# Kernel tuning notes

Hardware: AMD Instinct MI355X
Metric: run time of the kernel (lower is better)

Reference implementation:

```python
import jax, jax.numpy as jnp
import numpy as np
import math

D_MODEL = 2048
N_HEADS = 16
D_FF = 8192
SEQ = 2048
BATCH = 2
THETA = 10000.0
EPS = 1e-5


def _rope(x, pos):
    # x: [B, H, S, d_k] ; pos: [B, S] int
    d = x.shape[-1]
    inv_freq = 1.0 / (THETA ** (jnp.arange(0, d, 2, dtype=jnp.float32) / d))  # [d/2]
    ang = pos[..., None].astype(jnp.float32) * inv_freq  # [B, S, d/2]
    cos = jnp.cos(ang)[:, None, :, :, None]  # [B,1,S,d/2,1]
    sin = jnp.sin(ang)[:, None, :, :, None]
    xr = x.reshape(*x.shape[:-1], d // 2, 2)
    x1, x2 = xr[..., 0], xr[..., 1]
    rot = jnp.stack((-x2, x1), axis=-1)  # rotate pairs
    out = xr * cos + rot * sin
    return out.reshape(x.shape)


def _trunc_normal(key, shape, in_f, out_f):
    std = math.sqrt(2.0 / (in_f + out_f))
    return jax.random.truncated_normal(key, -3.0, 3.0, shape, jnp.float32) * std


def setup_inputs() -> dict:
    key = jax.random.key(0)
    ks = jax.random.split(key, 8)
    x = jax.random.normal(ks[0], (BATCH, SEQ, D_MODEL), jnp.float32)
    token_positions = jnp.sort(jax.random.randint(ks[1], (BATCH, SEQ), 0, SEQ), axis=-1)
    W_qkv = _trunc_normal(ks[2], (3 * D_MODEL, D_MODEL), D_MODEL, 3 * D_MODEL)
    W_o = _trunc_normal(ks[3], (D_MODEL, D_MODEL), D_MODEL, D_MODEL)
    W1 = _trunc_normal(ks[4], (D_FF, D_MODEL), D_MODEL, D_FF)
    W3 = _trunc_normal(ks[5], (D_FF, D_MODEL), D_MODEL, D_FF)
    W2 = _trunc_normal(ks[6], (D_MODEL, D_FF), D_FF, D_MODEL)
    g1 = jnp.ones((D_MODEL,), jnp.float32)
    g2 = jnp.ones((D_MODEL,), jnp.float32)
    return {"x": x, "token_positions": token_positions, "W_qkv": W_qkv, "W_o": W_o,
            "g1": g1, "g2": g2, "W1": W1, "W3": W3, "W2": W2}


def _rmsnorm(x, g):
    xf = x.astype(jnp.float32)
    rms = jnp.sqrt(jnp.mean(xf * xf, axis=-1, keepdims=True) + EPS)
    return (xf / rms * g).astype(x.dtype)


def reference(x, token_positions, W_qkv, W_o, g1, g2, W1, W3, W2):
    B, S, D = x.shape
    H = N_HEADS
    dk = D // H
    # --- attention sublayer ---
    h = _rmsnorm(x, g1)
    qkv = jnp.einsum('bsi,oi->bso', h, W_qkv)  # [B,S,3D]
    q, k, v = jnp.split(qkv, 3, axis=-1)
    to_heads = lambda t: t.reshape(B, S, H, dk).transpose(0, 2, 1, 3)  # [B,H,S,dk]
    q, k, v = to_heads(q), to_heads(k), to_heads(v)
    q = _rope(q, token_positions)
    k = _rope(k, token_positions)
    scores = jnp.einsum('bhnd,bhmd->bhnm', q, k) / math.sqrt(dk)  # [B,H,S,S]
    mask = jnp.tril(jnp.ones((S, S), dtype=bool))
    scores = jnp.where(mask, scores, -jnp.inf)
    attn = jax.nn.softmax(scores, axis=-1)
    o = jnp.einsum('bhnm,bhmd->bhnd', attn, v)
    o = o.transpose(0, 2, 1, 3).reshape(B, S, D)
    x = x + jnp.einsum('bsi,oi->bso', o, W_o)
    # --- SwiGLU FFN sublayer ---
    h2 = _rmsnorm(x, g2)
    x1 = jnp.einsum('bsi,oi->bso', h2, W1)
    x3 = jnp.einsum('bsi,oi->bso', h2, W3)
    x = x + jnp.einsum('bsi,oi->bso', jax.nn.silu(x1) * x3, W2)
    return x
```

## Files before the change

### kernel.cpp

```cpp
#include <hip/hip_runtime.h>

#define DEV __device__ __forceinline__

typedef __bf16 bf16x8 __attribute__((ext_vector_type(8)));
typedef float f32x4 __attribute__((ext_vector_type(4)));
typedef unsigned short u16x8 __attribute__((ext_vector_type(8)));
typedef unsigned short u16x2 __attribute__((ext_vector_type(2)));

DEV unsigned short f2bf(float f) {
  unsigned int u = __float_as_uint(f);
  u += 0x7fffu + ((u >> 16) & 1u);
  return (unsigned short)(u >> 16);
}
DEV float bf2f(unsigned short h) {
  return __uint_as_float(((unsigned int)h) << 16);
}
DEV void gload16(const void* g, void* l) {
  __builtin_amdgcn_global_load_lds(
      (const __attribute__((address_space(1))) unsigned int*)g,
      (__attribute__((address_space(3))) unsigned int*)l, 16, 0, 0);
}
DEV f32x4 mfma16(bf16x8 a, bf16x8 b, f32x4 c) {
  return __builtin_amdgcn_mfma_f32_16x16x32_bf16(a, b, c, 0, 0, 0);
}

#define SB   __builtin_amdgcn_s_barrier()
#define SCH  __builtin_amdgcn_sched_barrier(0)
#define LGKM0 asm volatile("s_waitcnt lgkmcnt(0)" ::: "memory")
#define LGKM4 asm volatile("s_waitcnt lgkmcnt(4)" ::: "memory")
#define VM6  asm volatile("s_waitcnt vmcnt(6)" ::: "memory")
#define PRIO1 __builtin_amdgcn_s_setprio(1)
#define PRIO0 __builtin_amdgcn_s_setprio(0)

__global__ __launch_bounds__(256) void k_cvt(const float* __restrict__ in,
                                             unsigned short* __restrict__ out, int n8) {
  const int stride = gridDim.x * 256;
  for (int i = blockIdx.x * 256 + threadIdx.x; i < n8; i += stride) {
    const float4* p = (const float4*)(in + (long)i * 8);
    const float4 a = p[0], b = p[1];
    u16x8 o = { f2bf(a.x), f2bf(a.y), f2bf(a.z), f2bf(a.w),
                f2bf(b.x), f2bf(b.y), f2bf(b.z), f2bf(b.w) };
    *(u16x8*)(out + (long)i * 8) = o;
  }
}

__global__ __launch_bounds__(256) void k_add(float* __restrict__ out,
                                             const float* __restrict__ p, int n4) {
  const int stride = gridDim.x * 256;
  for (int i = blockIdx.x * 256 + threadIdx.x; i < n4; i += stride) {
    float4 a = ((const float4*)out)[i];
    const float4 b = ((const float4*)p)[i];
    a.x += b.x; a.y += b.y; a.z += b.z; a.w += b.w;
    ((float4*)out)[i] = a;
  }
}

__global__ __launch_bounds__(256) void k_rmsnorm(const float* __restrict__ x,
                                                 const float* __restrict__ g,
                                                 unsigned short* __restrict__ out) {
  const int row = blockIdx.x;
  const int t = threadIdx.x;
  const float4* xr = (const float4*)(x + (long)row * 2048);
  const float4 a = xr[t * 2], c = xr[t * 2 + 1];
  float ss = a.x * a.x + a.y * a.y + a.z * a.z + a.w * a.w +
             c.x * c.x + c.y * c.y + c.z * c.z + c.w * c.w;
#pragma unroll
  for (int o = 32; o > 0; o >>= 1) ss += __shfl_down(ss, o);
  __shared__ float ws4[4];
  __shared__ float invs;
  if ((t & 63) == 0) ws4[t >> 6] = ss;
  __syncthreads();
  if (t == 0) invs = 1.0f / sqrtf((ws4[0] + ws4[1] + ws4[2] + ws4[3]) * (1.0f / 2048.0f) + 1e-5f);
  __syncthreads();
  const float inv = invs;
  const float4* gr = (const float4*)g;
  const float4 g0 = gr[t * 2], g1v = gr[t * 2 + 1];
  u16x8 o8 = { f2bf(a.x * inv * g0.x),  f2bf(a.y * inv * g0.y),
               f2bf(a.z * inv * g0.z),  f2bf(a.w * inv * g0.w),
               f2bf(c.x * inv * g1v.x), f2bf(c.y * inv * g1v.y),
               f2bf(c.z * inv * g1v.z), f2bf(c.w * inv * g1v.w) };
  *(u16x8*)(out + (long)row * 2048 + t * 8) = o8;
}

template <int EPI>
__global__ __launch_bounds__(512, 2) void k_gemm256(
    const unsigned short* __restrict__ A, const unsigned short* __restrict__ B,
    unsigned short* __restrict__ outBF, float* __restrict__ outF,
    const float* __restrict__ resid, const unsigned short* __restrict__ aux,
    float* __restrict__ partial, int M, int N, int K, int Keff) {
  __shared__ __align__(16) unsigned short lds[2][2][2][128][64];
  const int tid = threadIdx.x;
  const int wid = tid >> 6, lane = tid & 63;
  const int wr = wid >> 2, wc = wid & 3;
  const int fr = lane & 15, g4 = lane >> 4;

  const int nwg = gridDim.x;
  int bid = blockIdx.x;
  { int q = nwg >> 3, r = nwg & 7, xcd = bid & 7, lo = bid >> 3;
    bid = (xcd < r ? xcd * (q + 1) : r * (q + 1) + (xcd - r) * q) + lo; }
  int tile = bid, ks = 0;
  if constexpr (EPI == 3) { ks = bid & 1; tile = bid >> 1; }
  const int nxb = N >> 8;
  const int bx = tile % nxb, by = tile / nxb;
  const int arow0 = by << 8, bcol0 = bx << 8;
  const int NT = Keff >> 6;

  const int srow = tid >> 3;
  const int sg = (tid & 7) ^ (srow & 7);
  const unsigned short* Asrc = A + (long)(arow0 + srow) * K + (long)ks * Keff + (sg << 3);
  const unsigned short* Bsrc = B + (long)(bcol0 + srow) * K + (long)ks * Keff + (sg << 3);

  const int posk0 = (g4 ^ (lane & 7)) << 3;
  const int posk1 = ((4 + g4) ^ (lane & 7)) << 3;

  f32x4 acc[8][4] = {};
  bf16x8 a[4][2], b0[2][2], b1[2][2];

#define STAGE(SRC, xs, bufi, mat, h)                                            \
  { const unsigned short* s_ = (SRC) + (long)(h) * 128 * K + (long)(xs) * 64;   \
    unsigned short* d_ = &lds[bufi][mat][h][0][0] + wid * 512;                  \
    gload16(s_, d_);                                                            \
    gload16(s_ + (long)64 * K, d_ + 4096); }
#define RD_A(BA, mh)                                                            \
  _Pragma("unroll") for (int m_ = 0; m_ < 4; ++m_) {                            \
    const unsigned short* p_ = (BA) + ((mh) * 64 + m_ * 16 + fr) * 64;          \
    a[m_][0] = *(const bf16x8*)(p_ + posk0);                                    \
    a[m_][1] = *(const bf16x8*)(p_ + posk1); }
#define RD_B(BB, arr, nh)                                                       \
  _Pragma("unroll") for (int n_ = 0; n_ < 2; ++n_) {                            \
    const unsigned short* p_ = (BB) + ((nh) * 32 + n_ * 16 + fr) * 64;          \
    arr[n_][0] = *(const bf16x8*)(p_ + posk0);                                  \
    arr[n_][1] = *(const bf16x8*)(p_ + posk1); }
#define MM(mh, nh, Bv)                                                          \
  _Pragma("unroll") for (int k_ = 0; k_ < 2; ++k_)                              \
  _Pragma("unroll") for (int m_ = 0; m_ < 4; ++m_)                              \
  _Pragma("unroll") for (int n_ = 0; n_ < 2; ++n_)                              \
    acc[(mh)*4+m_][(nh)*2+n_] = mfma16(a[m_][k_], Bv[n_][k_], acc[(mh)*4+m_][(nh)*2+n_]);

  STAGE(Asrc, 0, 0, 0, 0);
  STAGE(Asrc, 0, 0, 0, 1);
  STAGE(Bsrc, 0, 0, 1, 0);
  STAGE(Bsrc, 0, 0, 1, 1);
  { const int x1p = (NT > 1) ? 1 : 0;
    STAGE(Bsrc, x1p, 1, 1, 0);
    STAGE(Bsrc, x1p, 1, 1, 1);
    STAGE(Asrc, x1p, 1, 0, 0); }
  VM6; SCH; SB; SCH;
  {
    const unsigned short* baseA = &lds[0][0][wr][0][0];
    const unsigned short* baseB = &lds[0][1][wc >> 1][0][0] + (wc & 1) * 4096;
    RD_A(baseA, 0); RD_B(baseB, b0, 0);
  }

  for (int t = 0; t < NT; ++t) {
    const unsigned short* baseA = &lds[t & 1][0][wr][0][0];
    const unsigned short* baseB = &lds[t & 1][1][wc >> 1][0][0] + (wc & 1) * 4096;
    const unsigned short* baseA2 = &lds[(t + 1) & 1][0][wr][0][0];
    const unsigned short* baseB2 = &lds[(t + 1) & 1][1][wc >> 1][0][0] + (wc & 1) * 4096;
    const int x1 = (t + 1 < NT) ? t + 1 : NT - 1;
    const int x2 = (t + 2 < NT) ? t + 2 : NT - 1;
    const int bn = (t + 1) & 1, bc = t & 1;

    SB;
    RD_B(baseB, b1, 1);
    STAGE(Asrc, x1, bn, 0, 1);
    LGKM4; SCH;
    PRIO1; MM(0, 0, b0); PRIO0;
    LGKM0; SCH;
    PRIO1; MM(0, 1, b1); PRIO0;

    SB;
    RD_A(baseA, 1);
    STAGE(Bsrc, x2, bc, 1, 0);
    LGKM0; SCH;
    PRIO1; MM(1, 1, b1); PRIO0;

    SB;
    STAGE(Asrc, x2, bc, 0, 0);
    STAGE(Bsrc, x2, bc, 1, 1);
    PRIO1; MM(1, 0, b0); PRIO0;
    VM6; SCH; SB; SCH;
    RD_A(baseA2, 0);
    RD_B(baseB2, b0, 0);
  }
#undef STAGE
#undef RD_A
#undef RD_B
#undef MM

  const int er = g4 << 2;
#pragma unroll
  for (int m = 0; m < 8; ++m) {
#pragma unroll
    for (int n = 0; n < 4; ++n) {
      const int grow = arow0 + wr * 128 + m * 16 + er;
      const int gcol = bcol0 + wc * 64 + n * 16 + fr;
#pragma unroll
      for (int r = 0; r < 4; ++r) {
        const long idx = (long)(grow + r) * N + gcol;
        const float v = acc[m][n][r];
        if constexpr (EPI == 0) {
          outBF[idx] = f2bf(v);
        } else if constexpr (EPI == 1) {
          outF[idx] = resid[idx] + v;
        } else if constexpr (EPI == 2) {
          const float x1v = bf2f(aux[idx]);
          const float sl = x1v / (1.0f + __expf(-x1v));
          outBF[idx] = f2bf(sl * v);
        } else {
          if (ks == 0) outF[idx] = resid[idx] + v;
          else         partial[idx] = v;
        }
      }
    }
  }
}

__global__ __launch_bounds__(512, 1) void k_gemm_n128(
    const unsigned short* __restrict__ A, const unsigned short* __restrict__ B,
    float* __restrict__ outF, const float* __restrict__ resid, int M, int N, int K) {
  __shared__ __align__(16) unsigned short lds[3][384 * 64];
  const int tid = threadIdx.x;
  const int wid = tid >> 6, lane = tid & 63;
  const int wr = wid >> 1, wc = wid & 1;
  const int fr = lane & 15, g4 = lane >> 4;

  const int nwg = gridDim.x;
  int bid = blockIdx.x;
  { int q = nwg >> 3, r = nwg & 7, xcd = bid & 7, lo = bid >> 3;
    bid = (xcd < r ? xcd * (q + 1) : r * (q + 1) + (xcd - r) * q) + lo; }
  const int nxb = N >> 7;
  const int bx = bid % nxb, by = bid / nxb;
  const int arow0 = by << 8, bcol0 = bx << 7;
  const int NT = K >> 6;

  const int srow = tid >> 3;
  const int sg = (tid & 7) ^ (srow & 7);
  const unsigned short* Asrc = A + (long)(arow0 + srow) * K + (sg << 3);
  const unsigned short* Bsrc = B + (long)(bcol0 + srow) * K + (sg << 3);

  const int posk0 = (g4 ^ (lane & 7)) << 3;
  const int posk1 = ((4 + g4) ^ (lane & 7)) << 3;

  f32x4 acc[4][4] = {};
  bf16x8 a[4][2], bl[2][2], bh[2][2];

#define SITE_A(xs, bufi, s)                                                    \
  gload16(Asrc + (long)((s) * 64) * K + (long)(xs) * 64,                       \
          &lds[bufi][(s) * 4096] + wid * 512);
#define SITE_B(xs, bufi, s)                                                    \
  gload16(Bsrc + (long)((s) * 64) * K + (long)(xs) * 64,                       \
          &lds[bufi][16384 + (s) * 4096] + wid * 512);
#define RDA(BUF)                                                               \
  _Pragma("unroll") for (int m_ = 0; m_ < 4; ++m_) {                           \
    const unsigned short* p_ = (BUF) + (wr * 64 + m_ * 16 + fr) * 64;          \
    a[m_][0] = *(const bf16x8*)(p_ + posk0);                                   \
    a[m_][1] = *(const bf16x8*)(p_ + posk1); }
#define RDB(BUF, arr, off)                                                     \
  _Pragma("unroll") for (int n_ = 0; n_ < 2; ++n_) {                           \
    const unsigned short* p_ = (BUF) + 16384 + (wc * 64 + (off) + n_ * 16 + fr) * 64; \
    arr[n_][0] = *(const bf16x8*)(p_ + posk0);                                 \
    arr[n_][1] = *(const bf16x8*)(p_ + posk1); }
#define MMN(nh, Bv)                                                            \
  _Pragma("unroll") for (int k_ = 0; k_ < 2; ++k_)                             \
  _Pragma("unroll") for (int m_ = 0; m_ < 4; ++m_)                             \
  _Pragma("unroll") for (int n_ = 0; n_ < 2; ++n_)                             \
    acc[m_][(nh)*2+n_] = mfma16(a[m_][k_], Bv[n_][k_], acc[m_][(nh)*2+n_]);

  SITE_A(0, 0, 0); SITE_A(0, 0, 1); SITE_A(0, 0, 2); SITE_A(0, 0, 3);
  SITE_B(0, 0, 0); SITE_B(0, 0, 1);
  { const int x1p = (NT > 1) ? 1 : 0;
    SITE_A(x1p, 1, 0); SITE_A(x1p, 1, 1); SITE_A(x1p, 1, 2); SITE_A(x1p, 1, 3);
    SITE_B(x1p, 1, 0); SITE_B(x1p, 1, 1); }
  VM6; SCH; SB; SCH;
  RDA(lds[0]); RDB(lds[0], bl, 0);

  for (int t = 0; t < NT; ++t) {
    const unsigned short* bufb = lds[t % 3];
    const unsigned short* bufn = lds[(t + 1) % 3];
    const int bn = (t + 2) % 3;
    const int xs = (t + 2 < NT) ? t + 2 : NT - 1;

    SB;
    RDB(bufb, bh, 32);
    SITE_A(xs, bn, 0); SITE_A(xs, bn, 1);
    LGKM4; SCH;
    PRIO1; MMN(0, bl); PRIO0;
    SITE_A(xs, bn, 2); SITE_A(xs, bn, 3); SITE_B(xs, bn, 0); SITE_B(xs, bn, 1);
    LGKM0; SCH;
    PRIO1; MMN(1, bh); PRIO0;
    VM6; SCH; SB; SCH;
    RDA(bufn); RDB(bufn, bl, 0);
  }
#undef SITE_A
#undef SITE_B
#undef RDA
#undef RDB
#undef MMN

  const int er = g4 << 2;
#pragma unroll
  for (int m = 0; m < 4; ++m) {
#pragma unroll
    for (int n = 0; n < 4; ++n) {
      const int grow = arow0 + wr * 64 + m * 16 + er;
      const int gcol = bcol0 + wc * 64 + n * 16 + fr;
#pragma unroll
      for (int r = 0; r < 4; ++r) {
        const long idx = (long)(grow + r) * N + gcol;
        outF[idx] = resid[idx] + acc[m][n][r];
      }
    }
  }
}

__global__ __launch_bounds__(256) void k_rope(const unsigned short* __restrict__ qkv,
                                              const int* __restrict__ tp,
                                              unsigned short* __restrict__ Qh,
                                              unsigned short* __restrict__ Kh, int S) {
  const int row = blockIdx.x;
  const int b = row / S, s = row - b * S;
  const float pos = (float)tp[row];
  for (int p = threadIdx.x; p < 1024; p += 256) {
    const int h = p >> 6, j = p & 63;
    const float ang = pos * __expf((float)j * -0.14391156831212787f);
    const float cc = cosf(ang), sn = sinf(ang);
    const long ib = (long)row * 6144 + h * 128 + (j << 1);
    const float q1 = bf2f(qkv[ib]), q2 = bf2f(qkv[ib + 1]);
    const float k1 = bf2f(qkv[ib + 2048]), k2v = bf2f(qkv[ib + 2049]);
    const long ob = (((long)(b * 16 + h)) * S + s) * 128 + (j << 1);
    u16x2 qo = { f2bf(q1 * cc - q2 * sn), f2bf(q2 * cc + q1 * sn) };
    u16x2 ko = { f2bf(k1 * cc - k2v * sn), f2bf(k2v * cc + k1 * sn) };
    *(u16x2*)&Qh[ob] = qo;
    *(u16x2*)&Kh[ob] = ko;
  }
}

__global__ __launch_bounds__(256) void k_vtrans(const unsigned short* __restrict__ qkv,
                                                unsigned short* __restrict__ Vt, int S) {
  __shared__ __align__(16) unsigned short t[128 * 72];
  const int bh = blockIdx.x, b = bh >> 4, h = bh & 15;
  const int s0 = blockIdx.y << 6;
  const int tid = threadIdx.x;
#pragma unroll
  for (int it = 0; it < 4; ++it) {
    const int sl = it * 16 + (tid >> 4);
    const int c = tid & 15;
    u16x8 v = *(const u16x8*)(qkv + ((long)(b * S + s0 + sl)) * 6144 + 4096 + h * 128 + (c << 3));
#pragma unroll
    for (int jj = 0; jj < 8; ++jj) t[(c * 8 + jj) * 72 + sl] = v[jj];
  }
  __syncthreads();
  const int d = tid >> 1, half = tid & 1;
  unsigned short* dst = Vt + ((long)bh * 128 + d) * S + s0 + half * 32;
  const unsigned short* srcr = &t[d * 72 + half * 32];
#pragma unroll
  for (int u = 0; u < 4; ++u)
    *(u16x8*)(dst + u * 8) = *(const u16x8*)(srcr + u * 8);
}

__global__ __launch_bounds__(256) void k_attn(const unsigned short* __restrict__ Q,
                                              const unsigned short* __restrict__ Kh,
                                              const unsigned short* __restrict__ Vt,
                                              unsigned short* __restrict__ O, int S) {
  __shared__ __align__(16) unsigned short lds_k[64 * 128];
  __shared__ __align__(16) unsigned short lds_v[128 * 64];
  __shared__ __align__(16) unsigned short lds_p[4 * 16 * 64];
  const int bh = blockIdx.x;
  const int b = bh >> 4, h = bh & 15;
  const int qt = gridDim.y - 1 - blockIdx.y;
  const int q0 = qt << 6;
  const int tid = threadIdx.x, w = tid >> 6, lane = tid & 63;
  const int fr = lane & 15, g4 = lane >> 4;

  bf16x8 qf[4];
  {
    const unsigned short* qb = Q + ((long)bh * S + q0 + w * 16 + fr) * 128 + (g4 << 3);
#pragma unroll
    for (int kk = 0; kk < 4; ++kk) qf[kk] = *(const bf16x8*)(qb + kk * 32);
  }

  f32x4 accO[8] = {};
  float mrow[4], lrow[4];
#pragma unroll
  for (int r = 0; r < 4; ++r) { mrow[r] = -1e30f; lrow[r] = 0.f; }

  const int k_row = (w << 4) + g4;
  const int k_cb = fr << 4;
  const int v_row = (w << 5) + (lane >> 3);
  const int v_cb = (lane & 7) << 4;
  const long kbase = (long)bh * S * 128;
  const long vbase = (long)bh * 128 * S;

  const int ntile = qt + 1;
  for (int it = 0; it < ntile; ++it) {
    const int kv0 = it << 6;
#pragma unroll
    for (int j = 0; j < 4; ++j) {
      const int kr = k_row + j * 4;
      const int kc = k_cb ^ ((kr & 7) << 4);
      gload16(Kh + kbase + (long)(kv0 + kr) * 128 + (kc >> 1), &lds_k[w * 2048 + j * 512]);
      const int vr = v_row + j * 8;
      const int vc = v_cb ^ ((vr & 7) << 4);
      gload16(Vt + vbase + (long)vr * S + kv0 + (vc >> 1), &lds_v[w * 2048 + j * 512]);
    }
    __syncthreads();

    f32x4 sc[4] = {};
#pragma unroll
    for (int kk = 0; kk < 4; ++kk) {
      const int kb = (kk << 6) + (g4 << 4);
#pragma unroll
      for (int n = 0; n < 4; ++n) {
        const int krw = n * 16 + fr;
        const int swz = (krw & 7) << 4;
        bf16x8 kf = *(const bf16x8*)&lds_k[krw * 128 + ((kb ^ swz) >> 1)];
        sc[n] = mfma16(qf[kk], kf, sc[n]);
      }
    }

    const float scl = 0.08838834764831845f;
    float sv[4][4];
    const bool needmask = (kv0 + 63 > q0 + w * 16);
#pragma unroll
    for (int n = 0; n < 4; ++n)
#pragma unroll
      for (int r = 0; r < 4; ++r) {
        float v = sc[n][r] * scl;
        if (needmask) {
          const int qi = q0 + w * 16 + (g4 << 2) + r;
          const int ki = kv0 + n * 16 + fr;
          if (ki > qi) v = -1e30f;
        }
        sv[n][r] = v;
      }
    float corr[4];
#pragma unroll
    for (int r = 0; r < 4; ++r) {
      float tm = fmaxf(fmaxf(sv[0][r], sv[1][r]), fmaxf(sv[2][r], sv[3][r]));
      tm = fmaxf(tm, __shfl_xor(tm, 1));
      tm = fmaxf(tm, __shfl_xor(tm, 2));
      tm = fmaxf(tm, __shfl_xor(tm, 4));
      tm = fmaxf(tm, __shfl_xor(tm, 8));
      const float mn = fmaxf(mrow[r], tm);
      corr[r] = __expf(mrow[r] - mn);
      mrow[r] = mn;
    }
    float rs[4] = {0.f, 0.f, 0.f, 0.f};
#pragma unroll
    for (int n = 0; n < 4; ++n)
#pragma unroll
      for (int r = 0; r < 4; ++r) {
        const float p = __expf(sv[n][r] - mrow[r]);
        rs[r] += p;
        const int pr = (g4 << 2) + r;
        const int pc = (n * 16 + fr) << 1;
        lds_p[(w << 10) + pr * 64 + ((pc ^ ((pr & 7) << 4)) >> 1)] = f2bf(p);
      }
#pragma unroll
    for (int r = 0; r < 4; ++r) {
      float s = rs[r];
      s += __shfl_xor(s, 1);
      s += __shfl_xor(s, 2);
      s += __shfl_xor(s, 4);
      s += __shfl_xor(s, 8);
      lrow[r] = lrow[r] * corr[r] + s;
    }
#pragma unroll
    for (int cb = 0; cb < 8; ++cb)
#pragma unroll
      for (int r = 0; r < 4; ++r) accO[cb][r] *= corr[r];

#pragma unroll
    for (int kk = 0; kk < 2; ++kk) {
      const int pb = (kk << 6) + (g4 << 4);
      bf16x8 pf = *(const bf16x8*)&lds_p[(w << 10) + fr * 64 + ((pb ^ ((fr & 7) << 4)) >> 1)];
#pragma unroll
      for (int cb = 0; cb < 8; ++cb) {
        const int vrw = cb * 16 + fr;
        bf16x8 vf = *(const bf16x8*)&lds_v[vrw * 64 + ((pb ^ ((vrw & 7) << 4)) >> 1)];
        accO[cb] = mfma16(pf, vf, accO[cb]);
      }
    }
    __syncthreads();
  }

#pragma unroll
  for (int cb = 0; cb < 8; ++cb)
#pragma unroll
    for (int r = 0; r < 4; ++r) {
      const int si = q0 + w * 16 + (g4 << 2) + r;
      const float o = accO[cb][r] / lrow[r];
      O[((long)b * S + si) * 2048 + h * 128 + cb * 16 + fr] = f2bf(o);
    }
}

extern "C" void kernel_launch(void* const* d_in, const int* in_sizes, int n_in,
                              void* d_out, int out_size, void* d_ws, size_t ws_size,
                              hipStream_t stream) {
  const float* x    = (const float*)d_in[0];
  const int*   tp   = (const int*)d_in[1];
  const float* Wqkv = (const float*)d_in[2];
  const float* Wo   = (const float*)d_in[3];
  const float* g1   = (const float*)d_in[4];
  const float* g2   = (const float*)d_in[5];
  const float* W1   = (const float*)d_in[6];
  const float* W3   = (const float*)d_in[7];
  const float* W2   = (const float*)d_in[8];
  float* out = (float*)d_out;

  char* ws = (char*)d_ws;
  const size_t MB = 1024 * 1024;
  unsigned short* Qh      = (unsigned short*)(ws + 0 * MB);
  unsigned short* Kh      = (unsigned short*)(ws + 16 * MB);
  unsigned short* Vt      = (unsigned short*)(ws + 32 * MB);
  unsigned short* O_bf    = (unsigned short*)(ws + 48 * MB);
  unsigned short* t_bf    = (unsigned short*)(ws + 0 * MB);
  unsigned short* qkv_bf  = (unsigned short*)(ws + 64 * MB);
  float*          x2      = (float*)         (ws + 64 * MB);
  unsigned short* h2_bf   = (unsigned short*)(ws + 96 * MB);
  unsigned short* wo_bf   = (unsigned short*)(ws + 96 * MB);
  unsigned short* wqkv_bf = (unsigned short*)(ws + 112 * MB);
  unsigned short* w1_bf   = (unsigned short*)(ws + 112 * MB);
  unsigned short* w2_bf   = (unsigned short*)(ws + 112 * MB);
  unsigned short* h1_bf   = (unsigned short*)(ws + 144 * MB);
  unsigned short* w3_bf   = (unsigned short*)(ws + 144 * MB);
  float*          part    = (float*)         (ws + 144 * MB);

  const int S = 2048;

  k_cvt<<<1024, 256, 0, stream>>>(Wqkv, wqkv_bf, 12582912 / 8);
  k_rmsnorm<<<4096, 256, 0, stream>>>(x, g1, h1_bf);
  k_gemm256<0><<<dim3(384), 512, 0, stream>>>(h1_bf, wqkv_bf, qkv_bf, nullptr, nullptr, nullptr, nullptr, 4096, 6144, 2048, 2048);
  k_rope<<<4096, 256, 0, stream>>>(qkv_bf, tp, Qh, Kh, S);
  k_vtrans<<<dim3(32, 32), 256, 0, stream>>>(qkv_bf, Vt, S);
  k_cvt<<<1024, 256, 0, stream>>>(Wo, wo_bf, 4194304 / 8);
  k_cvt<<<1024, 256, 0, stream>>>(W1, w1_bf, 16777216 / 8);
  k_cvt<<<1024, 256, 0, stream>>>(W3, w3_bf, 16777216 / 8);
  k_attn<<<dim3(32, 32), 256, 0, stream>>>(Qh, Kh, Vt, O_bf, S);
  k_gemm_n128<<<dim3(256), 512, 0, stream>>>(O_bf, wo_bf, x2, x, 4096, 2048, 2048);

  k_rmsnorm<<<4096, 256, 0, stream>>>(x2, g2, h2_bf);
  k_gemm256<0><<<dim3(512), 512, 0, stream>>>(h2_bf, w1_bf, t_bf, nullptr, nullptr, nullptr, nullptr, 4096, 8192, 2048, 2048);
  k_cvt<<<1024, 256, 0, stream>>>(W2, w2_bf, 16777216 / 8);
  k_gemm256<2><<<dim3(512), 512, 0, stream>>>(h2_bf, w3_bf, t_bf, nullptr, nullptr, t_bf, nullptr, 4096, 8192, 2048, 2048);
  k_gemm256<3><<<dim3(256), 512, 0, stream>>>(t_bf, w2_bf, nullptr, out, x2, nullptr, part, 4096, 2048, 8192, 4096);
  k_add<<<2048, 256, 0, stream>>>(out, part, 2097152);
}
```

Baseline: 752.0 us.

## Fuse RoPE and head split into QKV GEMM; split-K the Wo projection

The QKV GEMM gains an epilogue that applies RoPE to the Q and K columns and writes Q, K and V directly in per-head layout, which removes the separate rope kernel and the round trip through the qkv buffer. The V transpose now reads from the head-major V buffer. The Wo projection moves from a dedicated 128-wide GEMM to the 256-tile GEMM with split-K by two. The partial sum is folded into a new RMSNorm kernel that also writes the summed residual. The epilogue's scattered bf16 stores and per-element sincos may slow the GEMM tail, and split-K adds an extra fp32 partial write and read.

```diff
diff --git a/kernel.cpp b/kernel.cpp
--- a/kernel.cpp
+++ b/kernel.cpp
@@ -5,7 +5,6 @@
 typedef __bf16 bf16x8 __attribute__((ext_vector_type(8)));
 typedef float f32x4 __attribute__((ext_vector_type(4)));
 typedef unsigned short u16x8 __attribute__((ext_vector_type(8)));
-typedef unsigned short u16x2 __attribute__((ext_vector_type(2)));
 
 DEV unsigned short f2bf(float f) {
   unsigned int u = __float_as_uint(f);
@@ -82,12 +81,49 @@
   *(u16x8*)(out + (long)row * 2048 + t * 8) = o8;
 }
 
+__global__ __launch_bounds__(256) void k_rmsnorm2(const float* __restrict__ xa,
+                                                  const float* __restrict__ xb,
+                                                  const float* __restrict__ g,
+                                                  float* __restrict__ xsum,
+                                                  unsigned short* __restrict__ out) {
+  const int row = blockIdx.x;
+  const int t = threadIdx.x;
+  const float4* ar = (const float4*)(xa + (long)row * 2048);
+  const float4* br = (const float4*)(xb + (long)row * 2048);
+  float4 a = ar[t * 2], c = ar[t * 2 + 1];
+  const float4 pa = br[t * 2], pc = br[t * 2 + 1];
+  a.x += pa.x; a.y += pa.y; a.z += pa.z; a.w += pa.w;
+  c.x += pc.x; c.y += pc.y; c.z += pc.z; c.w += pc.w;
+  float4* sr = (float4*)(xsum + (long)row * 2048);
+  sr[t * 2] = a; sr[t * 2 + 1] = c;
+  float ss = a.x * a.x + a.y * a.y + a.z * a.z + a.w * a.w +
+             c.x * c.x + c.y * c.y + c.z * c.z + c.w * c.w;
+#pragma unroll
+  for (int o = 32; o > 0; o >>= 1) ss += __shfl_down(ss, o);
+  __shared__ float ws4[4];
+  __shared__ float invs;
+  if ((t & 63) == 0) ws4[t >> 6] = ss;
+  __syncthreads();
+  if (t == 0) invs = 1.0f / sqrtf((ws4[0] + ws4[1] + ws4[2] + ws4[3]) * (1.0f / 2048.0f) + 1e-5f);
+  __syncthreads();
+  const float inv = invs;
+  const float4* gr = (const float4*)g;
+  const float4 g0 = gr[t * 2], g1v = gr[t * 2 + 1];
+  u16x8 o8 = { f2bf(a.x * inv * g0.x),  f2bf(a.y * inv * g0.y),
+               f2bf(a.z * inv * g0.z),  f2bf(a.w * inv * g0.w),
+               f2bf(c.x * inv * g1v.x), f2bf(c.y * inv * g1v.y),
+               f2bf(c.z * inv * g1v.z), f2bf(c.w * inv * g1v.w) };
+  *(u16x8*)(out + (long)row * 2048 + t * 8) = o8;
+}
+
 template <int EPI>
 __global__ __launch_bounds__(512, 2) void k_gemm256(
     const unsigned short* __restrict__ A, const unsigned short* __restrict__ B,
     unsigned short* __restrict__ outBF, float* __restrict__ outF,
     const float* __restrict__ resid, const unsigned short* __restrict__ aux,
-    float* __restrict__ partial, int M, int N, int K, int Keff) {
+    float* __restrict__ partial, const int* __restrict__ tp,
+    unsigned short* __restrict__ p2, unsigned short* __restrict__ p3,
+    int M, int N, int K, int Keff) {
   __shared__ __align__(16) unsigned short lds[2][2][2][128][64];
   const int tid = threadIdx.x;
   const int wid = tid >> 6, lane = tid & 63;
@@ -158,7 +194,7 @@
     const unsigned short* baseA2 = &lds[(t + 1) & 1][0][wr][0][0];
     const unsigned short* baseB2 = &lds[(t + 1) & 1][1][wc >> 1][0][0] + (wc & 1) * 4096;
     const int x1 = (t + 1 < NT) ? t + 1 : NT - 1;
-    const int x2 = (t + 2 < NT) ? t + 2 : NT - 1;
+    const int x2i = (t + 2 < NT) ? t + 2 : NT - 1;
     const int bn = (t + 1) & 1, bc = t & 1;
 
     SB;
@@ -171,13 +207,13 @@
 
     SB;
     RD_A(baseA, 1);
-    STAGE(Bsrc, x2, bc, 1, 0);
+    STAGE(Bsrc, x2i, bc, 1, 0);
     LGKM0; SCH;
     PRIO1; MM(1, 1, b1); PRIO0;
 
     SB;
-    STAGE(Asrc, x2, bc, 0, 0);
-    STAGE(Bsrc, x2, bc, 1, 1);
+    STAGE(Asrc, x2i, bc, 0, 0);
+    STAGE(Bsrc, x2i, bc, 1, 1);
     PRIO1; MM(1, 0, b0); PRIO0;
     VM6; SCH; SB; SCH;
     RD_A(baseA2, 0);
@@ -189,166 +225,79 @@
 #undef MM
 
   const int er = g4 << 2;
-#pragma unroll
-  for (int m = 0; m < 8; ++m) {
-#pragma unroll
-    for (int n = 0; n < 4; ++n) {
+  if constexpr (EPI == 4) {
+    const int region = bcol0 >> 11;
+#pragma unroll
+    for (int m = 0; m < 8; ++m) {
       const int grow = arow0 + wr * 128 + m * 16 + er;
-      const int gcol = bcol0 + wc * 64 + n * 16 + fr;
-#pragma unroll
-      for (int r = 0; r < 4; ++r) {
-        const long idx = (long)(grow + r) * N + gcol;
-        const float v = acc[m][n][r];
-        if constexpr (EPI == 0) {
-          outBF[idx] = f2bf(v);
-        } else if constexpr (EPI == 1) {
-          outF[idx] = resid[idx] + v;
-        } else if constexpr (EPI == 2) {
-          const float x1v = bf2f(aux[idx]);
-          const float sl = x1v / (1.0f + __expf(-x1v));
-          outBF[idx] = f2bf(sl * v);
-        } else {
-          if (ks == 0) outF[idx] = resid[idx] + v;
-          else         partial[idx] = v;
+      float pos4[4];
+#pragma unroll
+      for (int r = 0; r < 4; ++r)
+        pos4[r] = (region < 2) ? (float)tp[grow + r] : 0.f;
+#pragma unroll
+      for (int n = 0; n < 4; ++n) {
+        const int gcol = bcol0 + wc * 64 + n * 16 + fr;
+        const int d = gcol & 127;
+        const float invf = __expf((float)(d >> 1) * -0.14391156831212787f);
+        const int h = (gcol >> 7) & 15;
+#pragma unroll
+        for (int r = 0; r < 4; ++r) {
+          const int row = grow + r;
+          const int b = row >> 11, s = row & 2047;
+          float v = acc[m][n][r];
+          if (region < 2) {
+            const float other = __shfl_xor(v, 1);
+            float cc, sn;
+            __sincosf(pos4[r] * invf, &sn, &cc);
+            v = (d & 1) ? (v * cc + other * sn) : (v * cc - other * sn);
+          }
+          unsigned short* dst = (region == 0) ? outBF : (region == 1 ? p2 : p3);
+          dst[((long)((b << 4) + h) * 2048 + s) * 128 + d] = f2bf(v);
         }
       }
     }
-  }
-}
-
-__global__ __launch_bounds__(512, 1) void k_gemm_n128(
-    const unsigned short* __restrict__ A, const unsigned short* __restrict__ B,
-    float* __restrict__ outF, const float* __restrict__ resid, int M, int N, int K) {
-  __shared__ __align__(16) unsigned short lds[3][384 * 64];
-  const int tid = threadIdx.x;
-  const int wid = tid >> 6, lane = tid & 63;
-  const int wr = wid >> 1, wc = wid & 1;
-  const int fr = lane & 15, g4 = lane >> 4;
-
-  const int nwg = gridDim.x;
-  int bid = blockIdx.x;
-  { int q = nwg >> 3, r = nwg & 7, xcd = bid & 7, lo = bid >> 3;
-    bid = (xcd < r ? xcd * (q + 1) : r * (q + 1) + (xcd - r) * q) + lo; }
-  const int nxb = N >> 7;
-  const int bx = bid % nxb, by = bid / nxb;
-  const int arow0 = by << 8, bcol0 = bx << 7;
-  const int NT = K >> 6;
-
-  const int srow = tid >> 3;
-  const int sg = (tid & 7) ^ (srow & 7);
-  const unsigned short* Asrc = A + (long)(arow0 + srow) * K + (sg << 3);
-  const unsigned short* Bsrc = B + (long)(bcol0 + srow) * K + (sg << 3);
-
-  const int posk0 = (g4 ^ (lane & 7)) << 3;
-  const int posk1 = ((4 + g4) ^ (lane & 7)) << 3;
-
-  f32x4 acc[4][4] = {};
-  bf16x8 a[4][2], bl[2][2], bh[2][2];
-
-#define SITE_A(xs, bufi, s)                                                    \
-  gload16(Asrc + (long)((s) * 64) * K + (long)(xs) * 64,                       \
-          &lds[bufi][(s) * 4096] + wid * 512);
-#define SITE_B(xs, bufi, s)                                                    \
-  gload16(Bsrc + (long)((s) * 64) * K + (long)(xs) * 64,                       \
-          &lds[bufi][16384 + (s) * 4096] + wid * 512);
-#define RDA(BUF)                                                               \
-  _Pragma("unroll") for (int m_ = 0; m_ < 4; ++m_) {                           \
-    const unsigned short* p_ = (BUF) + (wr * 64 + m_ * 16 + fr) * 64;          \
-    a[m_][0] = *(const bf16x8*)(p_ + posk0);                                   \
-    a[m_][1] = *(const bf16x8*)(p_ + posk1); }
-#define RDB(BUF, arr, off)                                                     \
-  _Pragma("unroll") for (int n_ = 0; n_ < 2; ++n_) {                           \
-    const unsigned short* p_ = (BUF) + 16384 + (wc * 64 + (off) + n_ * 16 + fr) * 64; \
-    arr[n_][0] = *(const bf16x8*)(p_ + posk0);                                 \
-    arr[n_][1] = *(const bf16x8*)(p_ + posk1); }
-#define MMN(nh, Bv)                                                            \
-  _Pragma("unroll") for (int k_ = 0; k_ < 2; ++k_)                             \
-  _Pragma("unroll") for (int m_ = 0; m_ < 4; ++m_)                             \
-  _Pragma("unroll") for (int n_ = 0; n_ < 2; ++n_)                             \
-    acc[m_][(nh)*2+n_] = mfma16(a[m_][k_], Bv[n_][k_], acc[m_][(nh)*2+n_]);
-
-  SITE_A(0, 0, 0); SITE_A(0, 0, 1); SITE_A(0, 0, 2); SITE_A(0, 0, 3);
-  SITE_B(0, 0, 0); SITE_B(0, 0, 1);
-  { const int x1p = (NT > 1) ? 1 : 0;
-    SITE_A(x1p, 1, 0); SITE_A(x1p, 1, 1); SITE_A(x1p, 1, 2); SITE_A(x1p, 1, 3);
-    SITE_B(x1p, 1, 0); SITE_B(x1p, 1, 1); }
-  VM6; SCH; SB; SCH;
-  RDA(lds[0]); RDB(lds[0], bl, 0);
-
-  for (int t = 0; t < NT; ++t) {
-    const unsigned short* bufb = lds[t % 3];
-    const unsigned short* bufn = lds[(t + 1) % 3];
-    const int bn = (t + 2) % 3;
-    const int xs = (t + 2 < NT) ? t + 2 : NT - 1;
-
-    SB;
-    RDB(bufb, bh, 32);
-    SITE_A(xs, bn, 0); SITE_A(xs, bn, 1);
-    LGKM4; SCH;
-    PRIO1; MMN(0, bl); PRIO0;
-    SITE_A(xs, bn, 2); SITE_A(xs, bn, 3); SITE_B(xs, bn, 0); SITE_B(xs, bn, 1);
-    LGKM0; SCH;
-    PRIO1; MMN(1, bh); PRIO0;
-    VM6; SCH; SB; SCH;
-    RDA(bufn); RDB(bufn, bl, 0);
-  }
-#undef SITE_A
-#undef SITE_B
-#undef RDA
-#undef RDB
-#undef MMN
-
-  const int er = g4 << 2;
-#pragma unroll
-  for (int m = 0; m < 4; ++m) {
-#pragma unroll
-    for (int n = 0; n < 4; ++n) {
-      const int grow = arow0 + wr * 64 + m * 16 + er;
-      const int gcol = bcol0 + wc * 64 + n * 16 + fr;
-#pragma unroll
-      for (int r = 0; r < 4; ++r) {
-        const long idx = (long)(grow + r) * N + gcol;
-        outF[idx] = resid[idx] + acc[m][n][r];
+  } else {
+#pragma unroll
+    for (int m = 0; m < 8; ++m) {
+#pragma unroll
+      for (int n = 0; n < 4; ++n) {
+        const int grow = arow0 + wr * 128 + m * 16 + er;
+        const int gcol = bcol0 + wc * 64 + n * 16 + fr;
+#pragma unroll
+        for (int r = 0; r < 4; ++r) {
+          const long idx = (long)(grow + r) * N + gcol;
+          const float v = acc[m][n][r];
+          if constexpr (EPI == 0) {
+            outBF[idx] = f2bf(v);
+          } else if constexpr (EPI == 1) {
+            outF[idx] = resid[idx] + v;
+          } else if constexpr (EPI == 2) {
+            const float x1v = bf2f(aux[idx]);
+            const float sl = x1v / (1.0f + __expf(-x1v));
+            outBF[idx] = f2bf(sl * v);
+          } else {
+            if (ks == 0) outF[idx] = resid[idx] + v;
+            else         partial[idx] = v;
+          }
+        }
       }
     }
   }
 }
 
-__global__ __launch_bounds__(256) void k_rope(const unsigned short* __restrict__ qkv,
-                                              const int* __restrict__ tp,
-                                              unsigned short* __restrict__ Qh,
-                                              unsigned short* __restrict__ Kh, int S) {
-  const int row = blockIdx.x;
-  const int b = row / S, s = row - b * S;
-  const float pos = (float)tp[row];
-  for (int p = threadIdx.x; p < 1024; p += 256) {
-    const int h = p >> 6, j = p & 63;
-    const float ang = pos * __expf((float)j * -0.14391156831212787f);
-    const float cc = cosf(ang), sn = sinf(ang);
-    const long ib = (long)row * 6144 + h * 128 + (j << 1);
-    const float q1 = bf2f(qkv[ib]), q2 = bf2f(qkv[ib + 1]);
-    const float k1 = bf2f(qkv[ib + 2048]), k2v = bf2f(qkv[ib + 2049]);
-    const long ob = (((long)(b * 16 + h)) * S + s) * 128 + (j << 1);
-    u16x2 qo = { f2bf(q1 * cc - q2 * sn), f2bf(q2 * cc + q1 * sn) };
-    u16x2 ko = { f2bf(k1 * cc - k2v * sn), f2bf(k2v * cc + k1 * sn) };
-    *(u16x2*)&Qh[ob] = qo;
-    *(u16x2*)&Kh[ob] = ko;
-  }
-}
-
-__global__ __launch_bounds__(256) void k_vtrans(const unsigned short* __restrict__ qkv,
+__global__ __launch_bounds__(256) void k_vtrans(const unsigned short* __restrict__ Vh,
                                                 unsigned short* __restrict__ Vt, int S) {
   __shared__ __align__(16) unsigned short t[128 * 72];
-  const int bh = blockIdx.x, b = bh >> 4, h = bh & 15;
+  const int bh = blockIdx.x;
   const int s0 = blockIdx.y << 6;
   const int tid = threadIdx.x;
+  const int sl = tid >> 2, c4 = tid & 3;
 #pragma unroll
   for (int it = 0; it < 4; ++it) {
-    const int sl = it * 16 + (tid >> 4);
-    const int c = tid & 15;
-    u16x8 v = *(const u16x8*)(qkv + ((long)(b * S + s0 + sl)) * 6144 + 4096 + h * 128 + (c << 3));
-#pragma unroll
-    for (int jj = 0; jj < 8; ++jj) t[(c * 8 + jj) * 72 + sl] = v[jj];
+    const int chunk = c4 * 4 + it;
+    u16x8 v = *(const u16x8*)(Vh + ((long)bh * S + s0 + sl) * 128 + chunk * 8);
+#pragma unroll
+    for (int jj = 0; jj < 8; ++jj) t[(chunk * 8 + jj) * 72 + sl] = v[jj];
   }
   __syncthreads();
   const int d = tid >> 1, half = tid & 1;
@@ -514,9 +463,9 @@
   unsigned short* Qh      = (unsigned short*)(ws + 0 * MB);
   unsigned short* Kh      = (unsigned short*)(ws + 16 * MB);
   unsigned short* Vt      = (unsigned short*)(ws + 32 * MB);
+  unsigned short* Vh      = (unsigned short*)(ws + 48 * MB);
   unsigned short* O_bf    = (unsigned short*)(ws + 48 * MB);
   unsigned short* t_bf    = (unsigned short*)(ws + 0 * MB);
-  unsigned short* qkv_bf  = (unsigned short*)(ws + 64 * MB);
   float*          x2      = (float*)         (ws + 64 * MB);
   unsigned short* h2_bf   = (unsigned short*)(ws + 96 * MB);
   unsigned short* wo_bf   = (unsigned short*)(ws + 96 * MB);
@@ -524,26 +473,30 @@
   unsigned short* w1_bf   = (unsigned short*)(ws + 112 * MB);
   unsigned short* w2_bf   = (unsigned short*)(ws + 112 * MB);
   unsigned short* h1_bf   = (unsigned short*)(ws + 144 * MB);
+  float*          part    = (float*)         (ws + 144 * MB);
   unsigned short* w3_bf   = (unsigned short*)(ws + 144 * MB);
-  float*          part    = (float*)         (ws + 144 * MB);
 
   const int S = 2048;
 
   k_cvt<<<1024, 256, 0, stream>>>(Wqkv, wqkv_bf, 12582912 / 8);
   k_rmsnorm<<<4096, 256, 0, stream>>>(x, g1, h1_bf);
-  k_gemm256<0><<<dim3(384), 512, 0, stream>>>(h1_bf, wqkv_bf, qkv_bf, nullptr, nullptr, nullptr, nullptr, 4096, 6144, 2048, 2048);
-  k_rope<<<4096, 256, 0, stream>>>(qkv_bf, tp, Qh, Kh, S);
-  k_vtrans<<<dim3(32, 32), 256, 0, stream>>>(qkv_bf, Vt, S);
+  k_gemm256<4><<<dim3(384), 512, 0, stream>>>(h1_bf, wqkv_bf, Qh, nullptr, nullptr, nullptr,
+                                              nullptr, tp, Kh, Vh, 4096, 6144, 2048, 2048);
+  k_vtrans<<<dim3(32, 32), 256, 0, stream>>>(Vh, Vt, S);
   k_cvt<<<1024, 256, 0, stream>>>(Wo, wo_bf, 4194304 / 8);
   k_cvt<<<1024, 256, 0, stream>>>(W1, w1_bf, 16777216 / 8);
+  k_attn<<<dim3(32, 32), 256, 0, stream>>>(Qh, Kh, Vt, O_bf, S);
+  k_gemm256<3><<<dim3(256), 512, 0, stream>>>(O_bf, wo_bf, nullptr, x2, x, nullptr,
+                                              part, nullptr, nullptr, nullptr, 4096, 2048, 2048, 1024);
+
+  k_rmsnorm2<<<4096, 256, 0, stream>>>(x2, part, g2, x2, h2_bf);
   k_cvt<<<1024, 256, 0, stream>>>(W3, w3_bf, 16777216 / 8);
-  k_attn<<<dim3(32, 32), 256, 0, stream>>>(Qh, Kh, Vt, O_bf, S);
-  k_gemm_n128<<<dim3(256), 512, 0, stream>>>(O_bf, wo_bf, x2, x, 4096, 2048, 2048);
-
-  k_rmsnorm<<<4096, 256, 0, stream>>>(x2, g2, h2_bf);
-  k_gemm256<0><<<dim3(512), 512, 0, stream>>>(h2_bf, w1_bf, t_bf, nullptr, nullptr, nullptr, nullptr, 4096, 8192, 2048, 2048);
+  k_gemm256<0><<<dim3(512), 512, 0, stream>>>(h2_bf, w1_bf, t_bf, nullptr, nullptr, nullptr,
+                                              nullptr, nullptr, nullptr, nullptr, 4096, 8192, 2048, 2048);
   k_cvt<<<1024, 256, 0, stream>>>(W2, w2_bf, 16777216 / 8);
-  k_gemm256<2><<<dim3(512), 512, 0, stream>>>(h2_bf, w3_bf, t_bf, nullptr, nullptr, t_bf, nullptr, 4096, 8192, 2048, 2048);
-  k_gemm256<3><<<dim3(256), 512, 0, stream>>>(t_bf, w2_bf, nullptr, out, x2, nullptr, part, 4096, 2048, 8192, 4096);
+  k_gemm256<2><<<dim3(512), 512, 0, stream>>>(h2_bf, w3_bf, t_bf, nullptr, nullptr, t_bf,
+                                              nullptr, nullptr, nullptr, nullptr, 4096, 8192, 2048, 2048);
+  k_gemm256<3><<<dim3(256), 512, 0, stream>>>(t_bf, w2_bf, nullptr, out, x2, nullptr,
+                                              part, nullptr, nullptr, nullptr, 4096, 2048, 8192, 4096);
   k_add<<<2048, 256, 0, stream>>>(out, part, 2097152);
 }
```

Result: slower. 807.2 us (+7.3%).
